# Performance work log

Hardware: AMD Instinct MI355X
Metric: run time of the kernel (lower is better)

The kernel has to match this reference:

```python
import jax, jax.numpy as jnp
import numpy as np

N, S, K, C_IN, C_OUT = 100000, 50000, 32, 128, 128


def setup_inputs() -> dict:
    key = jax.random.key(0)
    k1, k2, k3, k4, k5 = jax.random.split(key, 5)
    word_vec = jax.random.normal(k1, (N, C_IN), dtype=jnp.float32)
    # unique source indices (torch scatter-set with duplicate idx is nondeterministic)
    src_idx = jax.random.permutation(k2, N)[:S].astype(jnp.int64)
    neighs_idx = jax.random.randint(k3, (S, K), 0, N).astype(jnp.int64)
    src_mask = jax.random.randint(k4, (S, K), 0, 2).astype(jnp.int32)
    # xavier-uniform-style Linear weight, zero bias
    limit = float(np.sqrt(6.0 / (C_IN + C_OUT)))
    W_before = jax.random.uniform(k5, (C_OUT, C_IN), minval=-limit, maxval=limit, dtype=jnp.float32)
    b_before = jnp.zeros((C_OUT,), dtype=jnp.float32)
    return {"word_vec": word_vec, "src_idx": src_idx, "neighs_idx": neighs_idx,
            "src_mask": src_mask, "W_before": W_before, "b_before": b_before}


def reference(word_vec, src_idx, neighs_idx, src_mask, W_before, b_before):
    # dropout in eval mode -> identity
    supports = word_vec                                   # [N, C_in]
    q = supports[src_idx]                                 # [S, C_in]
    k = supports[neighs_idx]                              # [S, K, C_in]
    scores = jnp.einsum('sc,skc->sk', q, k) * 5.0         # [S, K]
    scores = jnp.where(src_mask == 1, scores, jnp.float32(-1e6))
    probs = jax.nn.softmax(scores, axis=-1)               # [S, K]
    # proj_before: Linear + LeakyReLU(0.2)
    supports = jax.nn.leaky_relu(word_vec @ W_before.T + b_before, negative_slope=0.2)  # [N, C_out]
    agg = jnp.einsum('sk,skc->sc', probs, supports[neighs_idx])  # [S, C_out]
    supports = supports.at[src_idx].set(agg)
    return supports
```

## Files before the change

kernel.cpp:

```cpp
#include <hip/hip_runtime.h>

#define NN 100000
#define SS 50000
#define KK 32
#define CC 128
#define RPB 160
#define LDA 136

typedef _Float16 f16x8 __attribute__((ext_vector_type(8)));
typedef _Float16 f16x4 __attribute__((ext_vector_type(4)));
typedef _Float16 f16x2 __attribute__((ext_vector_type(2)));
typedef float f32x4 __attribute__((ext_vector_type(4)));


__global__ __launch_bounds__(256) void proj_kernel(
    const float* __restrict__ wv,
    const float* __restrict__ W,
    const float* __restrict__ bias,
    _Float16* __restrict__ T,
    float* __restrict__ out)
{
    __shared__ _Float16 sA[RPB][LDA];

    const int t = threadIdx.x;
    const int base = blockIdx.x * RPB;

    #pragma unroll 4
    for (int i = 0; i < 20; i++) {
        const int idx = i * 256 + t;
        const int row = idx >> 5;
        const int c4 = (idx & 31) * 4;
        const float4 v = *(const float4*)(wv + (size_t)(base + row) * CC + c4);
        f16x4 h;
        h[0] = (_Float16)v.x; h[1] = (_Float16)v.y;
        h[2] = (_Float16)v.z; h[3] = (_Float16)v.w;
        *(f16x4*)&sA[row][c4] = h;
        *(f16x4*)(T + (size_t)(base + row) * 256 + c4) = h;
    }

    const int w = t >> 6;
    const int l = t & 63;
    const int q = l >> 4;
    const int c = l & 15;

    f16x8 bf[2][4];
    float bo[2];
    #pragma unroll
    for (int nch = 0; nch < 2; nch++) {
        const int n = w * 32 + nch * 16 + c;
        bo[nch] = bias[n];
        const float* Wr = W + (size_t)n * CC;
        #pragma unroll
        for (int kc = 0; kc < 4; kc++) {
            const int k0 = kc * 32 + q * 8;
            const float4 w0 = *(const float4*)(Wr + k0);
            const float4 w1 = *(const float4*)(Wr + k0 + 4);
            f16x8 b;
            b[0] = (_Float16)w0.x; b[1] = (_Float16)w0.y;
            b[2] = (_Float16)w0.z; b[3] = (_Float16)w0.w;
            b[4] = (_Float16)w1.x; b[5] = (_Float16)w1.y;
            b[6] = (_Float16)w1.z; b[7] = (_Float16)w1.w;
            bf[nch][kc] = b;
        }
    }
    __syncthreads();

    #pragma unroll 2
    for (int sub = 0; sub < RPB / 16; sub++) {
        const int rl = sub * 16 + c;

        f16x8 af[4];
        #pragma unroll
        for (int kc = 0; kc < 4; kc++)
            af[kc] = *(const f16x8*)&sA[rl][kc * 32 + q * 8];

        __syncthreads();

        f32x4 acc[2] = {{0.f, 0.f, 0.f, 0.f}, {0.f, 0.f, 0.f, 0.f}};
        #pragma unroll
        for (int kc = 0; kc < 4; kc++) {
            acc[0] = __builtin_amdgcn_mfma_f32_16x16x32_f16(af[kc], bf[0][kc], acc[0], 0, 0, 0);
            acc[1] = __builtin_amdgcn_mfma_f32_16x16x32_f16(af[kc], bf[1][kc], acc[1], 0, 0, 0);
        }

        #pragma unroll
        for (int nch = 0; nch < 2; nch++) {
            const int col = w * 32 + nch * 16 + c;
            #pragma unroll
            for (int rr = 0; rr < 4; rr++) {
                const int rowl = sub * 16 + q * 4 + rr;
                float v = acc[nch][rr] + bo[nch];
                v = v > 0.f ? v : 0.2f * v;
                out[(size_t)(base + rowl) * CC + col] = v;
                sA[rowl][col] = (_Float16)v;
            }
        }
    }

    __syncthreads();
    #pragma unroll 4
    for (int i = 0; i < 20; i++) {
        const int idx = i * 256 + t;
        const int row = idx >> 5;
        const int c4 = (idx & 31) * 4;
        *(f16x4*)(T + (size_t)(base + row) * 256 + 128 + c4) = *(const f16x4*)&sA[row][c4];
    }
}

__global__ __launch_bounds__(256, 4) void attn_kernel(
    const _Float16* __restrict__ T,
    const int* __restrict__ src_idx,
    const int* __restrict__ neighs,
    const int* __restrict__ mask,
    float* __restrict__ out)
{
    const int s = (blockIdx.x * 256 + threadIdx.x) >> 6;
    if (s >= SS) return;
    const int lane = threadIdx.x & 63;
    const int c = lane & 15;
    const int r = lane >> 4;

    int nbv[8];
    int mbits = 0;
    #pragma unroll
    for (int ch = 0; ch < 8; ch++) {
        nbv[ch] = neighs[s * KK + ch * 4 + r];
        mbits |= (mask[s * KK + ch * 4 + r] & 1) << ch;
    }
    const int src = src_idx[s];

    const bool havem = (__any(mbits) != 0);

    const char* Tb = (const char*)T;
    const unsigned cb = (unsigned)c << 4;

    unsigned off[8];
    #pragma unroll
    for (int ch = 0; ch < 8; ch++) {
        const int row = (((mbits >> ch) & 1) || !havem) ? nbv[ch] : src;
        off[ch] = ((unsigned)row << 9) + cb;
    }

    const f16x8 qh = *(const f16x8*)(Tb + (((unsigned)src << 9) + cb));
    f16x8 kh[8];
    #pragma unroll
    for (int ch = 0; ch < 8; ch++)
        kh[ch] = *(const f16x8*)(Tb + off[ch]);
    f16x8 vv[8];
    #pragma unroll
    for (int ch = 0; ch < 8; ch++)
        vv[ch] = *(const f16x8*)(Tb + off[ch] + 256);
    __builtin_amdgcn_sched_barrier(0);

    float sc[8];
    #pragma unroll
    for (int ch = 0; ch < 8; ch++) {
        float d = 0.f;
        #pragma unroll
        for (int j = 0; j < 4; j++) {
            f16x2 qa; qa[0] = qh[2 * j];     qa[1] = qh[2 * j + 1];
            f16x2 ka; ka[0] = kh[ch][2 * j]; ka[1] = kh[ch][2 * j + 1];
            d = __builtin_amdgcn_fdot2(qa, ka, d, false);
        }
        d += __shfl_xor(d, 1);
        d += __shfl_xor(d, 2);
        d += __shfl_xor(d, 4);
        d += __shfl_xor(d, 8);
        sc[ch] = ((mbits >> ch) & 1) ? d * 5.0f : -1e6f;
    }

    float mx = sc[0];
    #pragma unroll
    for (int ch = 1; ch < 8; ch++) mx = fmaxf(mx, sc[ch]);
    mx = fmaxf(mx, __shfl_xor(mx, 16));
    mx = fmaxf(mx, __shfl_xor(mx, 32));

    float p[8];
    float sum = 0.f;
    #pragma unroll
    for (int ch = 0; ch < 8; ch++) {
        p[ch] = __expf(sc[ch] - mx);
        sum += p[ch];
    }
    sum += __shfl_xor(sum, 16);
    sum += __shfl_xor(sum, 32);
    const float inv = __builtin_amdgcn_rcpf(sum);
    #pragma unroll
    for (int ch = 0; ch < 8; ch++) p[ch] *= inv;

    float acc[8] = {0.f, 0.f, 0.f, 0.f, 0.f, 0.f, 0.f, 0.f};
    #pragma unroll
    for (int ch = 0; ch < 8; ch++) {
        #pragma unroll
        for (int j = 0; j < 8; j++)
            acc[j] += p[ch] * (float)vv[ch][j];
    }

    #pragma unroll
    for (int j = 0; j < 8; j++) {
        acc[j] += __shfl_xor(acc[j], 16);
        acc[j] += __shfl_xor(acc[j], 32);
    }

    *((float2*)(out + (size_t)src * CC) + c * 4 + r) =
        make_float2(acc[r * 2], acc[r * 2 + 1]);
}

extern "C" void kernel_launch(void* const* d_in, const int* in_sizes, int n_in,
                              void* d_out, int out_size, void* d_ws, size_t ws_size,
                              hipStream_t stream)
{
    const float* wv   = (const float*)d_in[0];
    const int*   src  = (const int*)d_in[1];
    const int*   nei  = (const int*)d_in[2];
    const int*   msk  = (const int*)d_in[3];
    const float* W    = (const float*)d_in[4];
    const float* bias = (const float*)d_in[5];
    float* out = (float*)d_out;
    _Float16* T = (_Float16*)d_ws;

    proj_kernel<<<NN / RPB, 256, 0, stream>>>(wv, W, bias, T, out);
    attn_kernel<<<(SS * 64) / 256, 256, 0, stream>>>(T, src, nei, msk, out);
}
```

Before: 190.0 us.

## Write projected halves directly, ballot mask loads, raise attn occupancy, defer V loads

The projection kernel now writes its f16 output straight to the global T buffer. This removes a per-subtile __syncthreads and the final shared-memory copy pass, at the cost of scattered 2-byte global stores. The attention kernel loads neighbor indices and mask once per lane, then distributes them with ballot and shuffles instead of repeated global loads. Occupancy for the attention kernel goes from 4 to 8 waves per SIMD. The V-row loads are moved after the score computation, which lowers register pressure but exposes more memory latency per wave.

```diff
diff --git a/kernel.cpp b/kernel.cpp
--- a/kernel.cpp
+++ b/kernel.cpp
@@ -74,8 +74,6 @@
         for (int kc = 0; kc < 4; kc++)
             af[kc] = *(const f16x8*)&sA[rl][kc * 32 + q * 8];
 
-        __syncthreads();
-
         f32x4 acc[2] = {{0.f, 0.f, 0.f, 0.f}, {0.f, 0.f, 0.f, 0.f}};
         #pragma unroll
         for (int kc = 0; kc < 4; kc++) {
@@ -87,27 +85,18 @@
         for (int nch = 0; nch < 2; nch++) {
             const int col = w * 32 + nch * 16 + c;
             #pragma unroll
-            for (int rr = 0; rr < 4; rr++) {
-                const int rowl = sub * 16 + q * 4 + rr;
-                float v = acc[nch][rr] + bo[nch];
+            for (int r = 0; r < 4; r++) {
+                const int row = base + sub * 16 + q * 4 + r;
+                float v = acc[nch][r] + bo[nch];
                 v = v > 0.f ? v : 0.2f * v;
-                out[(size_t)(base + rowl) * CC + col] = v;
-                sA[rowl][col] = (_Float16)v;
+                out[(size_t)row * CC + col] = v;
+                T[(size_t)row * 256 + 128 + col] = (_Float16)v;
             }
         }
     }
-
-    __syncthreads();
-    #pragma unroll 4
-    for (int i = 0; i < 20; i++) {
-        const int idx = i * 256 + t;
-        const int row = idx >> 5;
-        const int c4 = (idx & 31) * 4;
-        *(f16x4*)(T + (size_t)(base + row) * 256 + 128 + c4) = *(const f16x4*)&sA[row][c4];
-    }
 }
 
-__global__ __launch_bounds__(256, 4) void attn_kernel(
+__global__ __launch_bounds__(256, 8) void attn_kernel(
     const _Float16* __restrict__ T,
     const int* __restrict__ src_idx,
     const int* __restrict__ neighs,
@@ -120,16 +109,20 @@
     const int c = lane & 15;
     const int r = lane >> 4;
 
-    int nbv[8];
-    int mbits = 0;
-    #pragma unroll
-    for (int ch = 0; ch < 8; ch++) {
-        nbv[ch] = neighs[s * KK + ch * 4 + r];
-        mbits |= (mask[s * KK + ch * 4 + r] & 1) << ch;
-    }
+    const int e = lane & 31;
+    const int nb_l = neighs[s * KK + e];
+    const int mk_l = mask[s * KK + e];
     const int src = src_idx[s];
 
-    const bool havem = (__any(mbits) != 0);
+    const unsigned long long mb = __ballot(mk_l == 1);
+    const bool havem = (mb != 0ull);
+
+    int nbv[8], mbits = 0;
+    #pragma unroll
+    for (int ch = 0; ch < 8; ch++) {
+        nbv[ch] = __shfl(nb_l, ch * 4 + r);
+        mbits |= (int)((mb >> (ch * 4 + r)) & 1ull) << ch;
+    }
 
     const char* Tb = (const char*)T;
     const unsigned cb = (unsigned)c << 4;
@@ -146,11 +139,6 @@
     #pragma unroll
     for (int ch = 0; ch < 8; ch++)
         kh[ch] = *(const f16x8*)(Tb + off[ch]);
-    f16x8 vv[8];
-    #pragma unroll
-    for (int ch = 0; ch < 8; ch++)
-        vv[ch] = *(const f16x8*)(Tb + off[ch] + 256);
-    __builtin_amdgcn_sched_barrier(0);
 
     float sc[8];
     #pragma unroll
@@ -168,6 +156,13 @@
         d += __shfl_xor(d, 8);
         sc[ch] = ((mbits >> ch) & 1) ? d * 5.0f : -1e6f;
     }
+
+    __builtin_amdgcn_sched_barrier(0);
+
+    f16x8 vv[8];
+    #pragma unroll
+    for (int ch = 0; ch < 8; ch++)
+        vv[ch] = *(const f16x8*)(Tb + off[ch] + 256);
 
     float mx = sc[0];
     #pragma unroll
```

Measured after the change: 190.9 us. No clear change (+0.5%).
